# Optimization experiments

Hardware: AMD Instinct MI355X
Metric: run time of the kernel (lower is better)

Reference implementation:

```python
import jax, jax.numpy as jnp
import numpy as np

B, S_BYTES = 8, 8192
NUM_EMB, BYTE_DIM = 384, 128
EMB_DIM = 1024
NUM_TOKENS = 2048
PAD_ID = 0
SCALE = BYTE_DIM ** 0.5


def setup_inputs() -> dict:
    key = jax.random.key(0)
    k1, k2, k3, k4 = jax.random.split(key, 4)
    x = jax.random.randint(k1, (B, S_BYTES), 0, NUM_EMB, dtype=jnp.int32)
    byte_groups = jnp.sort(
        jax.random.randint(k2, (B, S_BYTES), 0, NUM_TOKENS, dtype=jnp.int32), axis=-1
    )
    # TokenEmbedding init: normal std = byte_dim**-0.5, padding row zeroed
    emb_weight = jax.random.normal(k3, (NUM_EMB, BYTE_DIM), dtype=jnp.float32) * (BYTE_DIM ** -0.5)
    emb_weight = emb_weight.at[PAD_ID].set(0.0)
    # nn.Linear(byte_dim, emb_dim, bias=False): weight [out, in]
    out_proj_w = jax.random.normal(k4, (EMB_DIM, BYTE_DIM), dtype=jnp.float32) * (BYTE_DIM ** -0.5)
    return {"x": x, "byte_groups": byte_groups, "emb_weight": emb_weight, "out_proj_w": out_proj_w}


def _segment_mean(vals, segs):
    # vals: [S, D], segs: [S] sorted segment ids in [0, NUM_TOKENS)
    sums = jax.ops.segment_sum(vals, segs, num_segments=NUM_TOKENS)
    cnts = jax.ops.segment_sum(jnp.ones(segs.shape, vals.dtype), segs, num_segments=NUM_TOKENS)
    return sums / jnp.maximum(cnts, 1.0)[:, None]


def reference(x, byte_groups, emb_weight, out_proj_w):
    # embedding lookup with sqrt(dim) scale: [B, S_bytes, byte_dim]
    byte_emb = emb_weight[x] * jnp.asarray(SCALE, emb_weight.dtype)
    # ragged mean pooling over byte groups -> [B, NUM_TOKENS, byte_dim]
    grouped = jax.vmap(_segment_mean)(byte_emb, byte_groups)
    # out_proj (no bias) -> [B, NUM_TOKENS, emb_dim]; dropout inactive (p=0 / eval)
    emb = jnp.einsum("btd,ed->bte", grouped, out_proj_w)
    return emb
```

## Files before the change

### kernel.cpp

```cpp
#include <hip/hip_runtime.h>
#include <hip/hip_bf16.h>

#define BATCH      8
#define S_BYTES    8192
#define NUM_EMB    384
#define BYTE_DIM   128
#define EMB_DIM    1024
#define NUM_TOKENS 2048
#define SCALE_F    11.313708498984761f

#define M_TOTAL (BATCH * NUM_TOKENS)
#define SEG_STRIDE 2064

typedef __bf16 bf16x8 __attribute__((ext_vector_type(8)));
typedef float  floatx4 __attribute__((ext_vector_type(4)));

__global__ __launch_bounds__(256) void prep_kernel(
    const int* __restrict__ bg,
    int* __restrict__ seg,
    const float* __restrict__ w,
    __hip_bfloat16* __restrict__ wb)
{
    if (blockIdx.x < 256) {
        const int gid = blockIdx.x * 256 + threadIdx.x;
        const int b = gid >> 13;
        const int i = gid & (S_BYTES - 1);
        const int g  = bg[gid];
        const int gp = (i == 0) ? -1 : bg[gid - 1];
        int* __restrict__ srow = seg + b * SEG_STRIDE;
        for (int t = gp + 1; t <= g; ++t) srow[t] = i;
        if (i == S_BYTES - 1) {
            for (int t = g + 1; t <= NUM_TOKENS; ++t) srow[t] = S_BYTES;
        }
    } else {
        const int i = ((blockIdx.x - 256) * 256 + threadIdx.x) * 4;
        const float4 v = *(const float4*)(w + i);
        wb[i + 0] = __float2bfloat16(v.x);
        wb[i + 1] = __float2bfloat16(v.y);
        wb[i + 2] = __float2bfloat16(v.z);
        wb[i + 3] = __float2bfloat16(v.w);
    }
}

__global__ __launch_bounds__(128) void pool_kernel(
    const int* __restrict__ x,
    const int* __restrict__ seg,
    const float* __restrict__ emb,
    __hip_bfloat16* __restrict__ grouped)
{
    const int sub  = threadIdx.x >> 5;
    const int lane = threadIdx.x & 31;
    const int m    = blockIdx.x * 4 + sub;
    const int b    = m >> 11;
    const int t    = m & (NUM_TOKENS - 1);

    const int s   = seg[b * SEG_STRIDE + t];
    const int e   = seg[b * SEG_STRIDE + t + 1];
    const int cnt = e - s;

    const int* __restrict__ xrow = x + b * S_BYTES;
    const float4* __restrict__ embv = (const float4*)emb;

    float4 sum = {0.f, 0.f, 0.f, 0.f};
    #pragma unroll 4
    for (int i = s; i < e; ++i) {
        const int ei = xrow[i];
        const float4 v = embv[ei * 32 + lane];
        sum.x += v.x; sum.y += v.y; sum.z += v.z; sum.w += v.w;
    }
    const float inv = SCALE_F / (float)(cnt > 1 ? cnt : 1);

    __hip_bfloat16 o[4];
    o[0] = __float2bfloat16(sum.x * inv);
    o[1] = __float2bfloat16(sum.y * inv);
    o[2] = __float2bfloat16(sum.z * inv);
    o[3] = __float2bfloat16(sum.w * inv);
    *(uint2*)(grouped + (size_t)m * BYTE_DIM + lane * 4) = *(const uint2*)o;
}

__global__ __launch_bounds__(256) void gemm_kernel(
    const __hip_bfloat16* __restrict__ A,
    const __hip_bfloat16* __restrict__ W,
    float* __restrict__ out)
{
    __shared__ __hip_bfloat16 sA[128 * 128];
    __shared__ __hip_bfloat16 sB[128 * 128];

    const int mb = blockIdx.x & 127;
    const int nb = blockIdx.x >> 7;
    const int m0 = mb * 128;
    const int n0 = nb * 128;
    const int tid = threadIdx.x;

    {
        const bf16x8* __restrict__ gA = (const bf16x8*)(A + (size_t)m0 * BYTE_DIM);
        const bf16x8* __restrict__ gB = (const bf16x8*)(W + (size_t)n0 * BYTE_DIM);
        bf16x8* __restrict__ lA = (bf16x8*)sA;
        bf16x8* __restrict__ lB = (bf16x8*)sB;
        #pragma unroll
        for (int i = 0; i < 8; ++i) {
            lA[tid + i * 256] = gA[tid + i * 256];
            lB[tid + i * 256] = gB[tid + i * 256];
        }
    }
    __syncthreads();

    const int wave = tid >> 6;
    const int lane = tid & 63;
    const int wm = wave >> 1;
    const int wn = wave & 1;
    const int r    = lane & 15;
    const int quad = lane >> 4;

    floatx4 acc[4][4] = {};

    #pragma unroll
    for (int kk = 0; kk < 4; ++kk) {
        bf16x8 af[4], bfr[4];
        #pragma unroll
        for (int i = 0; i < 4; ++i)
            af[i] = *(const bf16x8*)(sA + (wm * 64 + i * 16 + r) * BYTE_DIM + kk * 32 + quad * 8);
        #pragma unroll
        for (int j = 0; j < 4; ++j)
            bfr[j] = *(const bf16x8*)(sB + (wn * 64 + j * 16 + r) * BYTE_DIM + kk * 32 + quad * 8);
        #pragma unroll
        for (int i = 0; i < 4; ++i)
            #pragma unroll
            for (int j = 0; j < 4; ++j)
                acc[i][j] = __builtin_amdgcn_mfma_f32_16x16x32_bf16(af[i], bfr[j], acc[i][j], 0, 0, 0);
    }

    #pragma unroll
    for (int i = 0; i < 4; ++i) {
        const int mrow = m0 + wm * 64 + i * 16 + quad * 4;
        #pragma unroll
        for (int j = 0; j < 4; ++j) {
            const int ncol = n0 + wn * 64 + j * 16 + r;
            float* __restrict__ p = out + (size_t)mrow * EMB_DIM + ncol;
            #pragma unroll
            for (int reg = 0; reg < 4; ++reg)
                p[(size_t)reg * EMB_DIM] = acc[i][j][reg];
        }
    }
}

extern "C" void kernel_launch(void* const* d_in, const int* in_sizes, int n_in,
                              void* d_out, int out_size, void* d_ws, size_t ws_size,
                              hipStream_t stream) {
    const int*   x   = (const int*)d_in[0];
    const int*   bg  = (const int*)d_in[1];
    const float* emb = (const float*)d_in[2];
    const float* w   = (const float*)d_in[3];
    float*       out = (float*)d_out;

    __hip_bfloat16* grouped = (__hip_bfloat16*)d_ws;
    __hip_bfloat16* wb      = (__hip_bfloat16*)((char*)d_ws + (size_t)M_TOTAL * BYTE_DIM * 2);
    int*            seg     = (int*)((char*)d_ws + (size_t)M_TOTAL * BYTE_DIM * 2
                                                 + (size_t)EMB_DIM * BYTE_DIM * 2);

    prep_kernel<<<256 + (EMB_DIM * BYTE_DIM) / (256 * 4), 256, 0, stream>>>(bg, seg, w, wb);
    pool_kernel<<<M_TOTAL / 4, 128, 0, stream>>>(x, seg, emb, grouped);
    gemm_kernel<<<(M_TOTAL / 128) * (EMB_DIM / 128), 256, 0, stream>>>(grouped, wb, out);
}
```

Before: 93.32 us.

## Project embedding table before pooling and fuse projection into prep kernel

Uses linearity to apply the output projection to the 384-row embedding table first, then mean-pools the projected 1024-wide rows per token directly into the output. The large per-token GEMM and the bf16 intermediate are removed, and the small GEMM is fused into the prep kernel. The cost is that pooling now gathers rows 8x wider, relying on the small projected table staying cache-resident. Output is written with nontemporal stores.

```diff
diff --git a/kernel.cpp b/kernel.cpp
--- a/kernel.cpp
+++ b/kernel.cpp
@@ -16,11 +16,15 @@
 typedef float  floatx4 __attribute__((ext_vector_type(4)));
 
 __global__ __launch_bounds__(256) void prep_kernel(
-    const int* __restrict__ bg,
-    int* __restrict__ seg,
+    const int*   __restrict__ bg,
+    int*         __restrict__ seg,
+    const float* __restrict__ emb,
     const float* __restrict__ w,
-    __hip_bfloat16* __restrict__ wb)
+    float*       __restrict__ proj)
 {
+    __shared__ __hip_bfloat16 sA[128 * 128];
+    __shared__ __hip_bfloat16 sB[128 * 128];
+
     if (blockIdx.x < 256) {
         const int gid = blockIdx.x * 256 + threadIdx.x;
         const int b = gid >> 13;
@@ -32,75 +36,32 @@
         if (i == S_BYTES - 1) {
             for (int t = g + 1; t <= NUM_TOKENS; ++t) srow[t] = S_BYTES;
         }
-    } else {
-        const int i = ((blockIdx.x - 256) * 256 + threadIdx.x) * 4;
-        const float4 v = *(const float4*)(w + i);
-        wb[i + 0] = __float2bfloat16(v.x);
-        wb[i + 1] = __float2bfloat16(v.y);
-        wb[i + 2] = __float2bfloat16(v.z);
-        wb[i + 3] = __float2bfloat16(v.w);
+        return;
     }
-}
 
-__global__ __launch_bounds__(128) void pool_kernel(
-    const int* __restrict__ x,
-    const int* __restrict__ seg,
-    const float* __restrict__ emb,
-    __hip_bfloat16* __restrict__ grouped)
-{
-    const int sub  = threadIdx.x >> 5;
-    const int lane = threadIdx.x & 31;
-    const int m    = blockIdx.x * 4 + sub;
-    const int b    = m >> 11;
-    const int t    = m & (NUM_TOKENS - 1);
-
-    const int s   = seg[b * SEG_STRIDE + t];
-    const int e   = seg[b * SEG_STRIDE + t + 1];
-    const int cnt = e - s;
-
-    const int* __restrict__ xrow = x + b * S_BYTES;
-    const float4* __restrict__ embv = (const float4*)emb;
-
-    float4 sum = {0.f, 0.f, 0.f, 0.f};
-    #pragma unroll 4
-    for (int i = s; i < e; ++i) {
-        const int ei = xrow[i];
-        const float4 v = embv[ei * 32 + lane];
-        sum.x += v.x; sum.y += v.y; sum.z += v.z; sum.w += v.w;
-    }
-    const float inv = SCALE_F / (float)(cnt > 1 ? cnt : 1);
-
-    __hip_bfloat16 o[4];
-    o[0] = __float2bfloat16(sum.x * inv);
-    o[1] = __float2bfloat16(sum.y * inv);
-    o[2] = __float2bfloat16(sum.z * inv);
-    o[3] = __float2bfloat16(sum.w * inv);
-    *(uint2*)(grouped + (size_t)m * BYTE_DIM + lane * 4) = *(const uint2*)o;
-}
-
-__global__ __launch_bounds__(256) void gemm_kernel(
-    const __hip_bfloat16* __restrict__ A,
-    const __hip_bfloat16* __restrict__ W,
-    float* __restrict__ out)
-{
-    __shared__ __hip_bfloat16 sA[128 * 128];
-    __shared__ __hip_bfloat16 sB[128 * 128];
-
-    const int mb = blockIdx.x & 127;
-    const int nb = blockIdx.x >> 7;
+    const int gb = blockIdx.x - 256;
+    const int mb = gb >> 3;
+    const int nb = gb & 7;
     const int m0 = mb * 128;
     const int n0 = nb * 128;
     const int tid = threadIdx.x;
 
     {
-        const bf16x8* __restrict__ gA = (const bf16x8*)(A + (size_t)m0 * BYTE_DIM);
-        const bf16x8* __restrict__ gB = (const bf16x8*)(W + (size_t)n0 * BYTE_DIM);
-        bf16x8* __restrict__ lA = (bf16x8*)sA;
-        bf16x8* __restrict__ lB = (bf16x8*)sB;
+        const float4* __restrict__ gA = (const float4*)(emb + (size_t)m0 * BYTE_DIM);
+        const float4* __restrict__ gB = (const float4*)(w   + (size_t)n0 * BYTE_DIM);
         #pragma unroll
-        for (int i = 0; i < 8; ++i) {
-            lA[tid + i * 256] = gA[tid + i * 256];
-            lB[tid + i * 256] = gB[tid + i * 256];
+        for (int i = 0; i < 16; ++i) {
+            const int idx = tid + i * 256;
+            const float4 a = gA[idx];
+            const float4 c = gB[idx];
+            alignas(8) __hip_bfloat16 ha[4] = {
+                __float2bfloat16(a.x), __float2bfloat16(a.y),
+                __float2bfloat16(a.z), __float2bfloat16(a.w)};
+            alignas(8) __hip_bfloat16 hb[4] = {
+                __float2bfloat16(c.x), __float2bfloat16(c.y),
+                __float2bfloat16(c.z), __float2bfloat16(c.w)};
+            *(uint2*)(sA + idx * 4) = *(const uint2*)ha;
+            *(uint2*)(sB + idx * 4) = *(const uint2*)hb;
         }
     }
     __syncthreads();
@@ -136,12 +97,42 @@
         #pragma unroll
         for (int j = 0; j < 4; ++j) {
             const int ncol = n0 + wn * 64 + j * 16 + r;
-            float* __restrict__ p = out + (size_t)mrow * EMB_DIM + ncol;
+            float* __restrict__ p = proj + (size_t)mrow * EMB_DIM + ncol;
             #pragma unroll
             for (int reg = 0; reg < 4; ++reg)
                 p[(size_t)reg * EMB_DIM] = acc[i][j][reg];
         }
     }
+}
+
+__global__ __launch_bounds__(256) void pool_kernel(
+    const int*   __restrict__ x,
+    const int*   __restrict__ seg,
+    const float* __restrict__ proj,
+    float*       __restrict__ out)
+{
+    const int m = blockIdx.x;
+    const int b = m >> 11;
+    const int t = m & (NUM_TOKENS - 1);
+
+    const int s   = seg[b * SEG_STRIDE + t];
+    const int e   = seg[b * SEG_STRIDE + t + 1];
+    const int cnt = e - s;
+
+    const int* __restrict__ xrow = x + b * S_BYTES;
+    const floatx4* __restrict__ pv = (const floatx4*)proj;
+
+    floatx4 acc = {0.f, 0.f, 0.f, 0.f};
+    #pragma unroll 4
+    for (int i = s; i < e; ++i) {
+        const int ei = xrow[i];
+        acc += pv[ei * 256 + threadIdx.x];
+    }
+
+    const float inv = SCALE_F / (float)(cnt > 1 ? cnt : 1);
+    acc *= inv;
+
+    __builtin_nontemporal_store(acc, (floatx4*)(out + (size_t)m * EMB_DIM) + threadIdx.x);
 }
 
 extern "C" void kernel_launch(void* const* d_in, const int* in_sizes, int n_in,
@@ -153,12 +144,9 @@
     const float* w   = (const float*)d_in[3];
     float*       out = (float*)d_out;
 
-    __hip_bfloat16* grouped = (__hip_bfloat16*)d_ws;
-    __hip_bfloat16* wb      = (__hip_bfloat16*)((char*)d_ws + (size_t)M_TOTAL * BYTE_DIM * 2);
-    int*            seg     = (int*)((char*)d_ws + (size_t)M_TOTAL * BYTE_DIM * 2
-                                                 + (size_t)EMB_DIM * BYTE_DIM * 2);
+    float* proj = (float*)d_ws;
+    int*   seg  = (int*)((char*)d_ws + (size_t)NUM_EMB * EMB_DIM * sizeof(float));
 
-    prep_kernel<<<256 + (EMB_DIM * BYTE_DIM) / (256 * 4), 256, 0, stream>>>(bg, seg, w, wb);
-    pool_kernel<<<M_TOTAL / 4, 128, 0, stream>>>(x, seg, emb, grouped);
-    gemm_kernel<<<(M_TOTAL / 128) * (EMB_DIM / 128), 256, 0, stream>>>(grouped, wb, out);
+    prep_kernel<<<256 + 24, 256, 0, stream>>>(bg, seg, emb, w, proj);
+    pool_kernel<<<M_TOTAL, 256, 0, stream>>>(x, seg, proj, out);
 }
```

Result: slower. 96.59 us (+3.5%).
